# Kernel optimization log

Measured on AMD Instinct MI355X. Metric: run time of the kernel, lower is better.

The kernel has to match this reference:

```python
import jax, jax.numpy as jnp
import numpy as np

B, S, DIN, DOUT = 4, 2048, 4096, 4096
W_SCALE = 64.0   # makes round(weight*scale) produce non-trivial int8 values
X_SCALE = 16.0   # input_scale so x*scale truncates to non-zero int32 values


def setup_inputs() -> dict:
    key = jax.random.key(0)
    k1, k2, k3 = jax.random.split(key, 3)
    # kaiming_uniform fan_in: bound = sqrt(6/fan_in)
    bound = float(np.sqrt(6.0 / DIN))
    weight = jax.random.uniform(k1, (DOUT, DIN), jnp.float32, -bound, bound)
    x = jax.random.normal(k2, (B, S, DIN), jnp.float32)
    bias = jax.random.normal(k3, (DOUT,), jnp.float32) * 0.01
    weight_scale = jnp.full((DOUT,), W_SCALE, jnp.float32)
    input_scale = jnp.full((1,), X_SCALE, jnp.float32)
    return {"x": x, "weight": weight, "bias": bias,
            "weight_scale": weight_scale, "input_scale": input_scale}


def reference(x, weight, bias, weight_scale, input_scale):
    # x = x * input_scale (pre-scale path of forward)
    xs = x * input_scale
    # fake-quant weights: round to int8 with wraparound, like torch .to(int8)
    w_int = jnp.round(weight * weight_scale[:, None]).astype(jnp.int8)
    # x.to(torch.int32): truncation toward zero
    x_int = xs.astype(jnp.int32)
    # F.linear on the integer-valued tensors (computed in f32: values are exact ints)
    acc = jnp.einsum('bsd,od->bso', x_int.astype(jnp.float32),
                     w_int.astype(jnp.float32))
    acc = acc + bias  # bias added inside linear
    # dequant: divide by per-channel weight_scale and the scalar input_scale
    out = acc / (weight_scale * input_scale)
    return out
```

## Files before the change

### kernel.cpp

```cpp
#include <hip/hip_runtime.h>

#define GM 8192
#define GN 4096
#define GK 4096

#define BM 128
#define BN 256
#define BK 64

using int4v = __attribute__((ext_vector_type(4))) int;

__global__ __launch_bounds__(256) void quant_x_k(const float4* __restrict__ x,
                                                 unsigned int* __restrict__ xq,
                                                 const float* __restrict__ iscale,
                                                 int n4) {
    int i = blockIdx.x * blockDim.x + threadIdx.x;
    if (i >= n4) return;
    float s = *iscale;
    float4 v = x[i];
    int q0 = (int)(v.x * s);
    int q1 = (int)(v.y * s);
    int q2 = (int)(v.z * s);
    int q3 = (int)(v.w * s);
    unsigned int packed = (unsigned int)(q0 & 0xff)
                        | ((unsigned int)(q1 & 0xff) << 8)
                        | ((unsigned int)(q2 & 0xff) << 16)
                        | ((unsigned int)(q3 & 0xff) << 24);
    xq[i] = packed;
}

__global__ __launch_bounds__(256) void quant_w_k(const float4* __restrict__ w,
                                                 unsigned int* __restrict__ wq,
                                                 const float* __restrict__ wscale,
                                                 int n4) {
    int i = blockIdx.x * blockDim.x + threadIdx.x;
    if (i >= n4) return;
    int row = i >> 10;
    float s = wscale[row];
    float4 v = w[i];
    int q0 = (int)rintf(v.x * s);
    int q1 = (int)rintf(v.y * s);
    int q2 = (int)rintf(v.z * s);
    int q3 = (int)rintf(v.w * s);
    unsigned int packed = (unsigned int)(q0 & 0xff)
                        | ((unsigned int)(q1 & 0xff) << 8)
                        | ((unsigned int)(q2 & 0xff) << 16)
                        | ((unsigned int)(q3 & 0xff) << 24);
    wq[i] = packed;
}

__global__ __launch_bounds__(256, 2) void qlinear_gemm_i8(
    const signed char* __restrict__ Aq,
    const signed char* __restrict__ Bq,
    const float* __restrict__ bias,
    const float* __restrict__ wscale,
    const float* __restrict__ iscale,
    float* __restrict__ C) {
    __shared__ signed char As[BM * BK];
    __shared__ signed char Bs[BN * BK];

    const int tid  = threadIdx.x;
    const int wave = tid >> 6;
    const int lane = tid & 63;
    const int m0 = blockIdx.x * BM;
    const int n0 = blockIdx.y * BN;
    const int wm = (wave >> 1) * 64;
    const int wn = (wave & 1) * 128;

    int4v acc[4][8];
#pragma unroll
    for (int i = 0; i < 4; ++i)
#pragma unroll
        for (int j = 0; j < 8; ++j)
            acc[i][j] = int4v{0, 0, 0, 0};

    const int kcl = (((lane & 3) ^ ((lane >> 3) & 3))) * 16;

    const int segA = wave * 2;
    const signed char* gA0 = Aq + (size_t)(m0 + segA * 16 + (lane >> 2)) * GK + kcl;
    signed char* lA0 = As + segA * 1024 + lane * 16;
    const int segB = wave * 4;
    const signed char* gB0 = Bq + (size_t)(n0 + segB * 16 + (lane >> 2)) * GK + kcl;
    signed char* lB0 = Bs + segB * 1024 + lane * 16;

    const int pos = ((lane >> 4) ^ ((lane >> 1) & 3)) * 16;
    const signed char* fA = As + (wm + (lane & 15)) * BK + pos;
    const signed char* fB = Bs + (wn + (lane & 15)) * BK + pos;

#define GLL16(g, l)                                                     \
    __builtin_amdgcn_global_load_lds(                                   \
        (__attribute__((address_space(1))) void*)(void*)(g),            \
        (__attribute__((address_space(3))) void*)(l), 16, 0, 0)

    for (int k0 = 0; k0 < GK; k0 += BK) {
        GLL16(gA0 + k0, lA0);
        GLL16(gA0 + (size_t)16 * GK + k0, lA0 + 1024);
        GLL16(gB0 + k0, lB0);
        GLL16(gB0 + (size_t)16 * GK + k0, lB0 + 1024);
        GLL16(gB0 + (size_t)32 * GK + k0, lB0 + 2048);
        GLL16(gB0 + (size_t)48 * GK + k0, lB0 + 3072);
        __syncthreads();

        int4v a[4], b[8];
#pragma unroll
        for (int i = 0; i < 4; ++i)
            a[i] = *(const int4v*)(fA + i * 16 * BK);
#pragma unroll
        for (int j = 0; j < 8; ++j)
            b[j] = *(const int4v*)(fB + j * 16 * BK);
#pragma unroll
        for (int mi = 0; mi < 4; ++mi)
#pragma unroll
            for (int ni = 0; ni < 8; ++ni)
                acc[mi][ni] = __builtin_amdgcn_mfma_i32_16x16x64_i8(
                    a[mi], b[ni], acc[mi][ni], 0, 0, 0);
        __syncthreads();
    }

    const float isc = *iscale;
#pragma unroll
    for (int ni = 0; ni < 8; ++ni) {
        const int col = n0 + wn + ni * 16 + (lane & 15);
        const float bs = bias[col];
        const float inv = 1.0f / (wscale[col] * isc);
#pragma unroll
        for (int mi = 0; mi < 4; ++mi) {
            const int row0 = m0 + wm + mi * 16 + (lane >> 4) * 4;
#pragma unroll
            for (int r = 0; r < 4; ++r) {
                C[(size_t)(row0 + r) * GN + col] =
                    ((float)acc[mi][ni][r] + bs) * inv;
            }
        }
    }
#undef GLL16
}

extern "C" void kernel_launch(void* const* d_in, const int* in_sizes, int n_in,
                              void* d_out, int out_size, void* d_ws, size_t ws_size,
                              hipStream_t stream) {
    const float* x      = (const float*)d_in[0];
    const float* w      = (const float*)d_in[1];
    const float* bias   = (const float*)d_in[2];
    const float* wscale = (const float*)d_in[3];
    const float* iscale = (const float*)d_in[4];
    float* out = (float*)d_out;

    signed char* xq = (signed char*)d_ws;
    signed char* wq = xq + (size_t)GM * GK;

    const int n4x = GM * GK / 4;
    quant_x_k<<<n4x / 256, 256, 0, stream>>>((const float4*)x,
                                             (unsigned int*)xq, iscale, n4x);
    const int n4w = GN * GK / 4;
    quant_w_k<<<n4w / 256, 256, 0, stream>>>((const float4*)w,
                                             (unsigned int*)wq, wscale, n4w);

    dim3 grid(GM / BM, GN / BN);
    qlinear_gemm_i8<<<grid, 256, 0, stream>>>(xq, wq, bias, wscale, iscale, out);
}
```

Baseline: 405.0 us.

## Triple-buffer LDS in int8 GEMM and merge quantization kernels

The GEMM main loop now uses a three-stage LDS ring. Async global-to-LDS loads for tile k+2 are issued before computing tile k, with a vmcnt wait and barrier placed once per iteration instead of two __syncthreads. MFMA sections also raise wave priority. Separately, the x and w quantization kernels are fused into one grid-stride launch. The extra buffering raises LDS use to about 72KB per block, which could limit occupancy, and the loop issues wasted wraparound loads on its last iterations.

```diff
diff --git a/kernel.cpp b/kernel.cpp
--- a/kernel.cpp
+++ b/kernel.cpp
@@ -7,46 +7,44 @@
 #define BM 128
 #define BN 256
 #define BK 64
+#define NT (GK / BK)
+#define ATILE (BM * BK)
+#define TILE_LDS (BM * BK + BN * BK)
 
 using int4v = __attribute__((ext_vector_type(4))) int;
 
-__global__ __launch_bounds__(256) void quant_x_k(const float4* __restrict__ x,
-                                                 unsigned int* __restrict__ xq,
-                                                 const float* __restrict__ iscale,
-                                                 int n4) {
-    int i = blockIdx.x * blockDim.x + threadIdx.x;
-    if (i >= n4) return;
-    float s = *iscale;
-    float4 v = x[i];
-    int q0 = (int)(v.x * s);
-    int q1 = (int)(v.y * s);
-    int q2 = (int)(v.z * s);
-    int q3 = (int)(v.w * s);
-    unsigned int packed = (unsigned int)(q0 & 0xff)
-                        | ((unsigned int)(q1 & 0xff) << 8)
-                        | ((unsigned int)(q2 & 0xff) << 16)
-                        | ((unsigned int)(q3 & 0xff) << 24);
-    xq[i] = packed;
-}
-
-__global__ __launch_bounds__(256) void quant_w_k(const float4* __restrict__ w,
-                                                 unsigned int* __restrict__ wq,
-                                                 const float* __restrict__ wscale,
-                                                 int n4) {
-    int i = blockIdx.x * blockDim.x + threadIdx.x;
-    if (i >= n4) return;
-    int row = i >> 10;
-    float s = wscale[row];
-    float4 v = w[i];
-    int q0 = (int)rintf(v.x * s);
-    int q1 = (int)rintf(v.y * s);
-    int q2 = (int)rintf(v.z * s);
-    int q3 = (int)rintf(v.w * s);
-    unsigned int packed = (unsigned int)(q0 & 0xff)
-                        | ((unsigned int)(q1 & 0xff) << 8)
-                        | ((unsigned int)(q2 & 0xff) << 16)
-                        | ((unsigned int)(q3 & 0xff) << 24);
-    wq[i] = packed;
+__global__ __launch_bounds__(256) void quant_xw_k(
+    const float4* __restrict__ x, unsigned int* __restrict__ xq,
+    const float4* __restrict__ w, unsigned int* __restrict__ wq,
+    const float* __restrict__ wscale, const float* __restrict__ iscale,
+    int n4x, int n4tot) {
+    const float xs = *iscale;
+    const int stride = gridDim.x * blockDim.x;
+    for (int i = blockIdx.x * blockDim.x + threadIdx.x; i < n4tot; i += stride) {
+        if (i < n4x) {
+            float4 v = x[i];
+            int q0 = (int)(v.x * xs);
+            int q1 = (int)(v.y * xs);
+            int q2 = (int)(v.z * xs);
+            int q3 = (int)(v.w * xs);
+            xq[i] = (unsigned int)(q0 & 0xff)
+                  | ((unsigned int)(q1 & 0xff) << 8)
+                  | ((unsigned int)(q2 & 0xff) << 16)
+                  | ((unsigned int)(q3 & 0xff) << 24);
+        } else {
+            int j = i - n4x;
+            float s = wscale[j >> 10];
+            float4 v = w[j];
+            int q0 = (int)rintf(v.x * s);
+            int q1 = (int)rintf(v.y * s);
+            int q2 = (int)rintf(v.z * s);
+            int q3 = (int)rintf(v.w * s);
+            wq[j] = (unsigned int)(q0 & 0xff)
+                  | ((unsigned int)(q1 & 0xff) << 8)
+                  | ((unsigned int)(q2 & 0xff) << 16)
+                  | ((unsigned int)(q3 & 0xff) << 24);
+        }
+    }
 }
 
 __global__ __launch_bounds__(256, 2) void qlinear_gemm_i8(
@@ -56,8 +54,7 @@
     const float* __restrict__ wscale,
     const float* __restrict__ iscale,
     float* __restrict__ C) {
-    __shared__ signed char As[BM * BK];
-    __shared__ signed char Bs[BN * BK];
+    __shared__ signed char smem[3][TILE_LDS];
 
     const int tid  = threadIdx.x;
     const int wave = tid >> 6;
@@ -75,46 +72,68 @@
             acc[i][j] = int4v{0, 0, 0, 0};
 
     const int kcl = (((lane & 3) ^ ((lane >> 3) & 3))) * 16;
-
     const int segA = wave * 2;
     const signed char* gA0 = Aq + (size_t)(m0 + segA * 16 + (lane >> 2)) * GK + kcl;
-    signed char* lA0 = As + segA * 1024 + lane * 16;
+    const int aoff = segA * 1024 + lane * 16;
     const int segB = wave * 4;
     const signed char* gB0 = Bq + (size_t)(n0 + segB * 16 + (lane >> 2)) * GK + kcl;
-    signed char* lB0 = Bs + segB * 1024 + lane * 16;
+    const int boff = ATILE + segB * 1024 + lane * 16;
 
     const int pos = ((lane >> 4) ^ ((lane >> 1) & 3)) * 16;
-    const signed char* fA = As + (wm + (lane & 15)) * BK + pos;
-    const signed char* fB = Bs + (wn + (lane & 15)) * BK + pos;
+    const int fAoff = (wm + (lane & 15)) * BK + pos;
+    const int fBoff = ATILE + (wn + (lane & 15)) * BK + pos;
 
 #define GLL16(g, l)                                                     \
     __builtin_amdgcn_global_load_lds(                                   \
         (__attribute__((address_space(1))) void*)(void*)(g),            \
-        (__attribute__((address_space(3))) void*)(l), 16, 0, 0)
+        (__attribute__((address_space(3))) void*)(void*)(l), 16, 0, 0)
 
-    for (int k0 = 0; k0 < GK; k0 += BK) {
-        GLL16(gA0 + k0, lA0);
-        GLL16(gA0 + (size_t)16 * GK + k0, lA0 + 1024);
-        GLL16(gB0 + k0, lB0);
-        GLL16(gB0 + (size_t)16 * GK + k0, lB0 + 1024);
-        GLL16(gB0 + (size_t)32 * GK + k0, lB0 + 2048);
-        GLL16(gB0 + (size_t)48 * GK + k0, lB0 + 3072);
-        __syncthreads();
+#define STAGE(kb, sb)                                                   \
+    do {                                                                \
+        GLL16(gA0 + (size_t)(kb), (sb) + aoff);                         \
+        GLL16(gA0 + (size_t)16 * GK + (kb), (sb) + aoff + 1024);        \
+        GLL16(gB0 + (size_t)(kb), (sb) + boff);                         \
+        GLL16(gB0 + (size_t)16 * GK + (kb), (sb) + boff + 1024);        \
+        GLL16(gB0 + (size_t)32 * GK + (kb), (sb) + boff + 2048);        \
+        GLL16(gB0 + (size_t)48 * GK + (kb), (sb) + boff + 3072);        \
+    } while (0)
 
+    STAGE(0, smem[0]);
+    STAGE(BK, smem[1]);
+    asm volatile("s_waitcnt vmcnt(6)" ::: "memory");
+    __builtin_amdgcn_s_barrier();
+    __builtin_amdgcn_sched_barrier(0);
+
+    int cur = 0;
+    int kstage = 2 * BK;
+    for (int t = 0; t < NT; ++t) {
+        int nb = cur + 2; if (nb >= 3) nb -= 3;
+        STAGE(kstage, smem[nb]);
+        kstage += BK; if (kstage >= GK) kstage = 0;
+        __builtin_amdgcn_sched_barrier(0);
+
+        const signed char* sb = smem[cur];
         int4v a[4], b[8];
 #pragma unroll
         for (int i = 0; i < 4; ++i)
-            a[i] = *(const int4v*)(fA + i * 16 * BK);
+            a[i] = *(const int4v*)(sb + fAoff + i * 16 * BK);
 #pragma unroll
         for (int j = 0; j < 8; ++j)
-            b[j] = *(const int4v*)(fB + j * 16 * BK);
+            b[j] = *(const int4v*)(sb + fBoff + j * 16 * BK);
+
+        __builtin_amdgcn_s_setprio(1);
 #pragma unroll
         for (int mi = 0; mi < 4; ++mi)
 #pragma unroll
             for (int ni = 0; ni < 8; ++ni)
                 acc[mi][ni] = __builtin_amdgcn_mfma_i32_16x16x64_i8(
                     a[mi], b[ni], acc[mi][ni], 0, 0, 0);
-        __syncthreads();
+        __builtin_amdgcn_s_setprio(0);
+
+        asm volatile("s_waitcnt vmcnt(6)" ::: "memory");
+        __builtin_amdgcn_s_barrier();
+        __builtin_amdgcn_sched_barrier(0);
+        cur += 1; if (cur == 3) cur = 0;
     }
 
     const float isc = *iscale;
@@ -133,6 +152,7 @@
             }
         }
     }
+#undef STAGE
 #undef GLL16
 }
 
@@ -150,11 +170,10 @@
     signed char* wq = xq + (size_t)GM * GK;
 
     const int n4x = GM * GK / 4;
-    quant_x_k<<<n4x / 256, 256, 0, stream>>>((const float4*)x,
-                                             (unsigned int*)xq, iscale, n4x);
     const int n4w = GN * GK / 4;
-    quant_w_k<<<n4w / 256, 256, 0, stream>>>((const float4*)w,
-                                             (unsigned int*)wq, wscale, n4w);
+    quant_xw_k<<<3072, 256, 0, stream>>>((const float4*)x, (unsigned int*)xq,
+                                         (const float4*)w, (unsigned int*)wq,
+                                         wscale, iscale, n4x, n4x + n4w);
 
     dim3 grid(GM / BM, GN / BN);
     qlinear_gemm_i8<<<grid, 256, 0, stream>>>(xq, wq, bias, wscale, iscale, out);
```

Result: no change. 400.6 us (-1.1%).
